# Optimization experiments

Hardware: AMD Instinct MI355X
Metric: run time of the kernel (lower is better)

The kernel has to match this reference:

```python
import jax, jax.numpy as jnp
import numpy as np


def setup_inputs() -> dict:
    key = jax.random.key(0)
    ks = jax.random.split(key, 10)
    B, D_X, D_H, D_S, D_T = 16384, 256, 512, 128, 128
    G = 4 * D_H
    sc = lambda d: 1.0 / np.sqrt(d)
    return {
        "x": jax.random.normal(ks[0], (B, D_X), jnp.float32),
        "h": jax.random.normal(ks[1], (B, D_H), jnp.float32),
        "c": jax.random.normal(ks[2], (B, D_H), jnp.float32),
        "spatial_per_step": jax.random.normal(ks[3], (B, D_S), jnp.float32),
        "temporal_per_step": jax.random.normal(ks[4], (B, D_T), jnp.float32),
        "W_x": jax.random.normal(ks[5], (D_X, G), jnp.float32) * sc(D_X),
        "W_h": jax.random.normal(ks[6], (D_H, G), jnp.float32) * sc(D_H),
        "b_h": jax.random.normal(ks[7], (G,), jnp.float32) * 0.01,
        "W_s": jax.random.normal(ks[8], (D_S, G), jnp.float32) * sc(D_S),
        "W_t": jax.random.normal(ks[9], (D_T, G), jnp.float32) * sc(D_T),
    }


def reference(x, h, c, spatial_per_step, temporal_per_step, W_x, W_h, b_h, W_s, W_t):
    H = W_h.shape[0]  # hidden_size
    # Four gate projections summed (the fusion opportunity): [B, 4H]
    preact = (x @ W_x) + (h @ W_h + b_h) + (spatial_per_step @ W_s) + (temporal_per_step @ W_t)
    i_g = jax.nn.sigmoid(preact[:, 0 * H:1 * H])
    f_g = jax.nn.sigmoid(preact[:, 1 * H:2 * H])
    o_g = jax.nn.sigmoid(preact[:, 2 * H:3 * H])
    c_g = jnp.tanh(preact[:, 3 * H:4 * H])
    c_new = f_g * c + i_g * c_g
    # NOTE: faithful to the source, h = tanh(o * c) (not o * tanh(c))
    h_new = jnp.tanh(o_g * c_new)
    return (h_new, c_new)
```

## Files before the change

kernel.cpp:

```cpp
#include <hip/hip_runtime.h>
#include <hip/hip_bf16.h>
#include <cstdint>

#define B_DIM 16384
#define DX 256
#define DH 512
#define DS 128
#define DT 128
#define KDIM 1024
#define NDIM 2048
#define HOUT 512

typedef __attribute__((ext_vector_type(8))) short short8;
typedef __attribute__((ext_vector_type(4))) float floatx4;

union bf16x8 {
  short8 v;
  __hip_bfloat16 b[8];
};

__device__ __forceinline__ float fast_sigmoid(float x) {
  return 1.f / (1.f + __expf(-x));
}
__device__ __forceinline__ float fast_tanh(float x) {
  float e = __expf(-2.f * x);
  return (1.f - e) / (1.f + e);
}


__global__ __launch_bounds__(256) void pack_AW(
    const float* __restrict__ x, const float* __restrict__ h,
    const float* __restrict__ sp_, const float* __restrict__ tp_,
    const float* __restrict__ Wx, const float* __restrict__ Wh,
    const float* __restrict__ Ws, const float* __restrict__ Wt,
    __hip_bfloat16* __restrict__ Ap, __hip_bfloat16* __restrict__ Wp) {
  const int NA = B_DIM * KDIM / 8 / 256;
  const int bid = blockIdx.x;
  if (bid < NA) {
    int tid = bid * 256 + threadIdx.x;
    int i = tid & 63;
    int t32 = (tid >> 6) & 31;
    int tile = tid >> 11;
    int kb = tile & 15, mb = tile >> 4;
    int s = t32 >> 4, c = t32 & 15;
    int row = c * 16 + (i >> 2);
    int kq = i & 3;
    int b = mb * 256 + row;
    int k = kb * 64 + s * 32 + kq * 8;
    const float* p;
    if (k < 768) {
      p = (k < 256) ? (x + (size_t)b * DX + k) : (h + (size_t)b * DH + (k - 256));
    } else {
      p = (k < 896) ? (sp_ + (size_t)b * DS + (k - 768))
                    : (tp_ + (size_t)b * DT + (k - 896));
    }
    floatx4 v0 = *(const floatx4*)p;
    floatx4 v1 = *(const floatx4*)(p + 4);
    bf16x8 o;
#pragma unroll
    for (int j = 0; j < 4; ++j) {
      o.b[j]     = __float2bfloat16(v0[j]);
      o.b[4 + j] = __float2bfloat16(v1[j]);
    }
    *(short8*)(Ap + (size_t)tid * 8) = o.v;
  } else {
    int tid = (bid - NA) * 256 + threadIdx.x;
    int i = tid & 63;
    int t16 = (tid >> 6) & 15;
    int tile = tid >> 10;
    int kb = tile & 15, nblk = tile >> 4;
    int s = t16 >> 3, c = t16 & 7;
    int pcol = c * 16 + (i >> 2);
    int kq = i & 3;
    int k = kb * 64 + s * 32 + kq * 8;
    int wn = pcol >> 6, g = (pcol >> 4) & 3, hl = pcol & 15;
    int col = g * 512 + nblk * 32 + wn * 16 + hl;
    const float* src; int kl;
    if (k < 256)      { src = Wx; kl = k; }
    else if (k < 768) { src = Wh; kl = k - 256; }
    else if (k < 896) { src = Ws; kl = k - 768; }
    else              { src = Wt; kl = k - 896; }
    bf16x8 o;
#pragma unroll
    for (int r = 0; r < 8; ++r)
      o.b[r] = __float2bfloat16(src[(size_t)(kl + r) * NDIM + col]);
    *(short8*)(Wp + (size_t)tid * 8) = o.v;
  }
}

#define LOADP(Af, Bf, p) do {                                          \
    const __hip_bfloat16* ap_ = aT + (size_t)(p) * 8192;               \
    const __hip_bfloat16* bp_ = bT + (size_t)(p) * 4096;               \
    _Pragma("unroll")                                                  \
    for (int mi_ = 0; mi_ < 8; ++mi_)                                  \
      Af[mi_] = *(const short8*)(ap_ + mi_ * 512);                     \
    _Pragma("unroll")                                                  \
    for (int ni_ = 0; ni_ < 4; ++ni_)                                  \
      Bf[ni_] = *(const short8*)(bp_ + ni_ * 512);                     \
  } while (0)

#define MFMAP(Af, Bf) do {                                             \
    _Pragma("unroll")                                                  \
    for (int mi_ = 0; mi_ < 8; ++mi_)                                  \
      _Pragma("unroll")                                                \
      for (int ni_ = 0; ni_ < 4; ++ni_)                                \
        acc[mi_][ni_] = __builtin_amdgcn_mfma_f32_16x16x32_bf16(       \
            Af[mi_], Bf[ni_], acc[mi_][ni_], 0, 0, 0);                 \
  } while (0)

__global__ __launch_bounds__(256, 2) void lstm_gemm(
    const __hip_bfloat16* __restrict__ Ap, const __hip_bfloat16* __restrict__ Wp,
    const float* __restrict__ bh, const float* __restrict__ c_in,
    float* __restrict__ out) {
  const int tid = threadIdx.x;
  const int lane = tid & 63;
  const int wid = tid >> 6;
  const int wm = wid & 1;
  const int wn = wid >> 1;
  const int q = lane >> 4;
  const int fr = lane & 15;

  const int bid = blockIdx.x;
  const int wg = (bid & 7) * 128 + (bid >> 3);
  const int mb = wg >> 4;
  const int nblk = wg & 15;
  const int m0 = mb * 256;

  const int ls = (fr * 4 + q) * 8;
  const __hip_bfloat16* aT =
      Ap + (size_t)mb * 262144 + (wm * 8) * 512 + ls;
  const __hip_bfloat16* bT =
      Wp + (size_t)nblk * 131072 + (wn * 4) * 512 + ls;

  floatx4 acc[8][4];
#pragma unroll
  for (int i = 0; i < 8; ++i)
#pragma unroll
    for (int j = 0; j < 4; ++j) acc[i][j] = (floatx4)0.f;

  short8 aP[8], bP[4], aQ[8], bQ[4];
  LOADP(aP, bP, 0);
  for (int p = 0; p < 30; p += 2) {
    LOADP(aQ, bQ, p + 1);
    MFMAP(aP, bP);
    LOADP(aP, bP, p + 2);
    MFMAP(aQ, bQ);
  }
  LOADP(aQ, bQ, 31);
  MFMAP(aP, bP);
  MFMAP(aQ, bQ);

  const int hh = nblk * 32 + wn * 16 + fr;
  float bias[4];
#pragma unroll
  for (int g = 0; g < 4; ++g) bias[g] = bh[g * 512 + hh];

#pragma unroll
  for (int mi = 0; mi < 8; ++mi) {
#pragma unroll
    for (int r = 0; r < 4; ++r) {
      const size_t grow = (size_t)(m0 + wm * 128 + mi * 16 + q * 4 + r);
      const float pi = acc[mi][0][r] + bias[0];
      const float pf = acc[mi][1][r] + bias[1];
      const float po = acc[mi][2][r] + bias[2];
      const float pc = acc[mi][3][r] + bias[3];
      const float ig = fast_sigmoid(pi);
      const float fg = fast_sigmoid(pf);
      const float og = fast_sigmoid(po);
      const float cg = fast_tanh(pc);
      const float cc = fg * c_in[grow * HOUT + hh] + ig * cg;
      out[grow * HOUT + hh] = fast_tanh(og * cc);
      out[(size_t)B_DIM * HOUT + grow * HOUT + hh] = cc;
    }
  }
}

extern "C" void kernel_launch(void* const* d_in, const int* in_sizes, int n_in,
                              void* d_out, int out_size, void* d_ws, size_t ws_size,
                              hipStream_t stream) {
  const float* x  = (const float*)d_in[0];
  const float* h  = (const float*)d_in[1];
  const float* c  = (const float*)d_in[2];
  const float* sp = (const float*)d_in[3];
  const float* tp = (const float*)d_in[4];
  const float* Wx = (const float*)d_in[5];
  const float* Wh = (const float*)d_in[6];
  const float* bh = (const float*)d_in[7];
  const float* Ws = (const float*)d_in[8];
  const float* Wt = (const float*)d_in[9];
  float* out = (float*)d_out;

  __hip_bfloat16* Ap = (__hip_bfloat16*)d_ws;
  __hip_bfloat16* Wp = (__hip_bfloat16*)((char*)d_ws + (size_t)B_DIM * KDIM * 2);

  const int nblk_A = B_DIM * KDIM / 8 / 256;
  const int nblk_W = NDIM * KDIM / 8 / 256;
  pack_AW<<<dim3(nblk_A + nblk_W), dim3(256), 0, stream>>>(
      x, h, sp, tp, Wx, Wh, Ws, Wt, Ap, Wp);
  lstm_gemm<<<dim3(1024), dim3(256), 0, stream>>>(Ap, Wp, bh, c, out);
}
```

Before: 272.1 us.

## Stage A tiles in LDS via async global_load_lds with triple buffering

The GEMM now uses 512-thread blocks covering 256x256 output tiles. The shared A panel is staged into a triple-buffered LDS ring with global_load_lds, and each wave keeps its own B fragments in registers. The A pack layout gets an XOR swizzle to avoid LDS bank conflicts, and the W pack layout is reorganised so each wave's B stream is contiguous. The intent is to stop every wave reloading A from global memory, cutting global traffic, at the cost of barriers per k-step and more LDS and register pressure.

```diff
diff --git a/kernel.cpp b/kernel.cpp
--- a/kernel.cpp
+++ b/kernel.cpp
@@ -10,6 +10,9 @@
 #define KDIM 1024
 #define NDIM 2048
 #define HOUT 512
+
+#define NT 32
+#define APAN 8192
 
 typedef __attribute__((ext_vector_type(8))) short short8;
 typedef __attribute__((ext_vector_type(4))) float floatx4;
@@ -44,7 +47,7 @@
     int kb = tile & 15, mb = tile >> 4;
     int s = t32 >> 4, c = t32 & 15;
     int row = c * 16 + (i >> 2);
-    int kq = i & 3;
+    int kq = (i & 3) ^ ((row >> 1) & 3);
     int b = mb * 256 + row;
     int k = kb * 64 + s * 32 + kq * 8;
     const float* p;
@@ -65,21 +68,18 @@
     *(short8*)(Ap + (size_t)tid * 8) = o.v;
   } else {
     int tid = (bid - NA) * 256 + threadIdx.x;
-    int i = tid & 63;
-    int t16 = (tid >> 6) & 15;
-    int tile = tid >> 10;
-    int kb = tile & 15, nblk = tile >> 4;
-    int s = t16 >> 3, c = t16 & 7;
-    int pcol = c * 16 + (i >> 2);
-    int kq = i & 3;
-    int k = kb * 64 + s * 32 + kq * 8;
-    int wn = pcol >> 6, g = (pcol >> 4) & 3, hl = pcol & 15;
-    int col = g * 512 + nblk * 32 + wn * 16 + hl;
+    int lane = tid & 63;
+    int g    = (tid >> 6) & 3;
+    int t    = (tid >> 8) & 31;
+    int wn   = (tid >> 13) & 3;
+    int nb   = (tid >> 15) & 7;
+    int col  = g * 512 + nb * 64 + wn * 16 + (lane & 15);
+    int kbase = t * 32 + (lane >> 4) * 8;
     const float* src; int kl;
-    if (k < 256)      { src = Wx; kl = k; }
-    else if (k < 768) { src = Wh; kl = k - 256; }
-    else if (k < 896) { src = Ws; kl = k - 768; }
-    else              { src = Wt; kl = k - 896; }
+    if (kbase < 256)      { src = Wx; kl = kbase; }
+    else if (kbase < 768) { src = Wh; kl = kbase - 256; }
+    else if (kbase < 896) { src = Ws; kl = kbase - 768; }
+    else                  { src = Wt; kl = kbase - 896; }
     bf16x8 o;
 #pragma unroll
     for (int r = 0; r < 8; ++r)
@@ -88,30 +88,65 @@
   }
 }
 
-#define LOADP(Af, Bf, p) do {                                          \
-    const __hip_bfloat16* ap_ = aT + (size_t)(p) * 8192;               \
-    const __hip_bfloat16* bp_ = bT + (size_t)(p) * 4096;               \
-    _Pragma("unroll")                                                  \
-    for (int mi_ = 0; mi_ < 8; ++mi_)                                  \
-      Af[mi_] = *(const short8*)(ap_ + mi_ * 512);                     \
-    _Pragma("unroll")                                                  \
-    for (int ni_ = 0; ni_ < 4; ++ni_)                                  \
-      Bf[ni_] = *(const short8*)(bp_ + ni_ * 512);                     \
+#define GLD(src, dst)                                              \
+  __builtin_amdgcn_global_load_lds(                                \
+      (const __attribute__((address_space(1))) void*)(src),        \
+      (__attribute__((address_space(3))) void*)(dst), 16, 0, 0)
+
+#define LOADB(B, tt) do {                                          \
+    const __hip_bfloat16* bp_ = bBase + (size_t)(tt) * 2048;       \
+    B[0] = *(const short8*)(bp_);                                  \
+    B[1] = *(const short8*)(bp_ + 512);                            \
+    B[2] = *(const short8*)(bp_ + 1024);                           \
+    B[3] = *(const short8*)(bp_ + 1536);                           \
   } while (0)
 
-#define MFMAP(Af, Bf) do {                                             \
-    _Pragma("unroll")                                                  \
-    for (int mi_ = 0; mi_ < 8; ++mi_)                                  \
-      _Pragma("unroll")                                                \
-      for (int ni_ = 0; ni_ < 4; ++ni_)                                \
-        acc[mi_][ni_] = __builtin_amdgcn_mfma_f32_16x16x32_bf16(       \
-            Af[mi_], Bf[ni_], acc[mi_][ni_], 0, 0, 0);                 \
+#define TILE(cur, nxt, t) do {                                               \
+    const unsigned short* Ar = As + sR * APAN;                               \
+    const int tb = ((t) + 1 < NT) ? (t) + 1 : NT - 1;                        \
+    const int ta = ((t) + 2 < NT) ? (t) + 2 : NT - 1;                        \
+    LOADB(nxt, tb);                      \
+    __builtin_amdgcn_sched_barrier(0);                                       \
+    const __hip_bfloat16* aP = aStg + (size_t)ta * APAN;                     \
+    GLD(aP, &As[sS * APAN + dA]);                                            \
+    GLD(aP + 512, &As[sS * APAN + dA + 512]);                                \
+    short8 a0[4];                                                            \
+    _Pragma("unroll")                                                        \
+    for (int i_ = 0; i_ < 4; ++i_) a0[i_] = *(const short8*)(Ar + aOff[i_]); \
+    asm volatile("s_barrier" ::: "memory");                                  \
+    __builtin_amdgcn_sched_barrier(0);                                       \
+    __builtin_amdgcn_s_setprio(1);                                           \
+    _Pragma("unroll")                                                        \
+    for (int mi_ = 0; mi_ < 4; ++mi_)                                        \
+      _Pragma("unroll")                                                      \
+      for (int g_ = 0; g_ < 4; ++g_)                                         \
+        acc[mi_][g_] = __builtin_amdgcn_mfma_f32_16x16x32_bf16(              \
+            a0[mi_], cur[g_], acc[mi_][g_], 0, 0, 0);                        \
+    __builtin_amdgcn_s_setprio(0);                                           \
+    short8 a1[4];                                                            \
+    _Pragma("unroll")                                                        \
+    for (int i_ = 0; i_ < 4; ++i_)                                           \
+      a1[i_] = *(const short8*)(Ar + aOff[4 + i_]);                          \
+    asm volatile("s_waitcnt vmcnt(2)\n\ts_barrier" ::: "memory");            \
+    __builtin_amdgcn_sched_barrier(0);                                       \
+    __builtin_amdgcn_s_setprio(1);                                           \
+    _Pragma("unroll")                                                        \
+    for (int mi_ = 0; mi_ < 4; ++mi_)                                        \
+      _Pragma("unroll")                                                      \
+      for (int g_ = 0; g_ < 4; ++g_)                                         \
+        acc[4 + mi_][g_] = __builtin_amdgcn_mfma_f32_16x16x32_bf16(          \
+            a1[mi_], cur[g_], acc[4 + mi_][g_], 0, 0, 0);                    \
+    __builtin_amdgcn_s_setprio(0);                                           \
+    sR = (sR == 2) ? 0 : sR + 1;                                             \
+    sS = (sS == 2) ? 0 : sS + 1;                                             \
   } while (0)
 
-__global__ __launch_bounds__(256, 2) void lstm_gemm(
+__global__ __launch_bounds__(512, 2) void lstm_gemm(
     const __hip_bfloat16* __restrict__ Ap, const __hip_bfloat16* __restrict__ Wp,
     const float* __restrict__ bh, const float* __restrict__ c_in,
     float* __restrict__ out) {
+  __shared__ unsigned short As[3 * APAN];
+
   const int tid = threadIdx.x;
   const int lane = tid & 63;
   const int wid = tid >> 6;
@@ -121,16 +156,17 @@
   const int fr = lane & 15;
 
   const int bid = blockIdx.x;
-  const int wg = (bid & 7) * 128 + (bid >> 3);
-  const int mb = wg >> 4;
-  const int nblk = wg & 15;
+  const int wg = (bid & 7) * 64 + (bid >> 3);
+  const int mb = wg >> 3;
+  const int nb = wg & 7;
   const int m0 = mb * 256;
 
-  const int ls = (fr * 4 + q) * 8;
-  const __hip_bfloat16* aT =
-      Ap + (size_t)mb * 262144 + (wm * 8) * 512 + ls;
-  const __hip_bfloat16* bT =
-      Wp + (size_t)nblk * 131072 + (wn * 4) * 512 + ls;
+  int aOff[8];
+#pragma unroll
+  for (int m = 0; m < 8; ++m) {
+    int row = wm * 128 + m * 16 + fr;
+    aOff[m] = row * 32 + (q ^ ((row >> 1) & 3)) * 8;
+  }
 
   floatx4 acc[8][4];
 #pragma unroll
@@ -138,19 +174,32 @@
 #pragma unroll
     for (int j = 0; j < 4; ++j) acc[i][j] = (floatx4)0.f;
 
-  short8 aP[8], bP[4], aQ[8], bQ[4];
-  LOADP(aP, bP, 0);
-  for (int p = 0; p < 30; p += 2) {
-    LOADP(aQ, bQ, p + 1);
-    MFMAP(aP, bP);
-    LOADP(aP, bP, p + 2);
-    MFMAP(aQ, bQ);
-  }
-  LOADP(aQ, bQ, 31);
-  MFMAP(aP, bP);
-  MFMAP(aQ, bQ);
-
-  const int hh = nblk * 32 + wn * 16 + fr;
+  const int ch0 = wid * 2;
+  const __hip_bfloat16* aStg = Ap + (size_t)mb * 262144 + ch0 * 512 + lane * 8;
+  const int dA = ch0 * 512;
+
+  const __hip_bfloat16* bBase =
+      Wp + (size_t)(nb * 4 + wn) * 65536 + (size_t)lane * 8;
+
+  short8 bA[4], bB[4];
+
+  LOADB(bA, 0);
+  __builtin_amdgcn_sched_barrier(0);
+  GLD(aStg, &As[dA]);
+  GLD(aStg + 512, &As[dA + 512]);
+  GLD(aStg + APAN, &As[APAN + dA]);
+  GLD(aStg + APAN + 512, &As[APAN + dA + 512]);
+  asm volatile("s_waitcnt vmcnt(2)\n\ts_barrier" ::: "memory");
+
+  int sR = 0;
+  int sS = 2;
+
+  for (int t = 0; t < NT; t += 2) {
+    TILE(bA, bB, t);
+    TILE(bB, bA, t + 1);
+  }
+
+  const int hh = nb * 64 + wn * 16 + fr;
   float bias[4];
 #pragma unroll
   for (int g = 0; g < 4; ++g) bias[g] = bh[g * 512 + hh];
@@ -197,5 +246,5 @@
   const int nblk_W = NDIM * KDIM / 8 / 256;
   pack_AW<<<dim3(nblk_A + nblk_W), dim3(256), 0, stream>>>(
       x, h, sp, tp, Wx, Wh, Ws, Wt, Ap, Wp);
-  lstm_gemm<<<dim3(1024), dim3(256), 0, stream>>>(Ap, Wp, bh, c, out);
-}
+  lstm_gemm<<<dim3(512), dim3(512), 0, stream>>>(Ap, Wp, bh, c, out);
+}
```

Measured after the change: 235.4 us. 1.16x faster.
